# Optimization experiments

Hardware: AMD Instinct MI355X
Metric: run time of the kernel (lower is better)

## Reference

```python
import jax, jax.numpy as jnp
import numpy as np

SP_NEAR = 2
BN_EPS = 1e-5


def setup_inputs() -> dict:
    key = jax.random.key(0)
    ks = jax.random.split(key, 8)
    bs, n_stk, n_stk_pnt, coord = 32, 32, 64, 32
    sp_in, sp_out, dn_in, dn_out = 1024, 512, 256, 128
    return {
        "sparse_fea": jax.random.normal(ks[0], (bs, sp_in, n_stk), jnp.float32),
        "dense_fea": jax.random.normal(ks[1], (bs, dn_in, n_stk, n_stk_pnt), jnp.float32),
        "stk_coor": jax.random.normal(ks[2], (bs, n_stk, coord), jnp.float32),
        "stk_coor_bef": jax.random.normal(ks[3], (bs, 2 * n_stk, coord), jnp.float32),
        "sp_w": jax.random.normal(ks[4], (sp_out, sp_in), jnp.float32) * 0.02,
        "sp_b": jnp.zeros((sp_out,), jnp.float32),
        "sp_gamma": jnp.ones((sp_out,), jnp.float32),
        "sp_beta": jnp.zeros((sp_out,), jnp.float32),
        "ct_w": jax.random.normal(ks[5], (dn_in, dn_out, 1, 4), jnp.float32) * 0.02,  # torch ConvTranspose2d layout [in,out,kh,kw]
        "ct_b": jnp.zeros((dn_out,), jnp.float32),
        "bn_gamma": jnp.ones((dn_out,), jnp.float32),
        "bn_beta": jnp.zeros((dn_out,), jnp.float32),
    }


def reference(sparse_fea, dense_fea, stk_coor, stk_coor_bef,
              sp_w, sp_b, sp_gamma, sp_beta, ct_w, ct_b, bn_gamma, bn_beta):
    bs, dn_in, n_stk, n_stk_pnt = dense_fea.shape
    n_bef = stk_coor_bef.shape[1]  # n_stk * 2

    # ---- squared pairwise distances [bs, n_bef, n_stk] (eu.square_distance) ----
    d = (jnp.sum(stk_coor_bef ** 2, -1)[:, :, None]
         + jnp.sum(stk_coor ** 2, -1)[:, None, :]
         - 2.0 * jnp.einsum('bnc,bmc->bnm', stk_coor_bef, stk_coor))

    # ---- k smallest distances (sort + slice == top_k of -d) ----
    neg_d, idx = jax.lax.top_k(-d, SP_NEAR)  # idx: [bs, n_bef, 2]
    dists = -neg_d

    # ---- inverse-distance interpolation weights ----
    dist_recip = 1.0 / (dists + 1e-8)
    weight = dist_recip / jnp.sum(dist_recip, axis=2, keepdims=True)  # [bs, n_bef, 2]

    # ---- sparse branch: gather [bs, c, n_bef, 2] then weighted sum over neighbors ----
    sp_g = jax.vmap(lambda f, i: f[:, i])(sparse_fea, idx)  # [bs, sp_in, n_bef, 2]
    sp_interp = jnp.einsum('bcnk,bnk->bcn', sp_g, weight)   # [bs, sp_in, n_bef]

    # eu.MLP(dim=1): Conv1d(k=1) + BatchNorm1d (batch stats) + ReLU (dropout = identity)
    h = jnp.einsum('oc,bcn->bon', sp_w, sp_interp) + sp_b[None, :, None]
    mu = h.mean(axis=(0, 2), keepdims=True)
    var = h.var(axis=(0, 2), keepdims=True)
    sparse_out = jax.nn.relu(sp_gamma[None, :, None] * (h - mu) * jax.lax.rsqrt(var + BN_EPS)
                             + sp_beta[None, :, None])

    # ---- dense branch: rearrange 'b c s sp -> b s (sp c)', gather, weighted sum ----
    dflat = jnp.transpose(dense_fea, (0, 2, 3, 1)).reshape(bs, n_stk, n_stk_pnt * dn_in)
    dg = jax.vmap(lambda f, i: f[i])(dflat, idx)            # [bs, n_bef, 2, sp*c]
    dsum = jnp.einsum('bnkd,bnk->bnd', dg, weight)          # [bs, n_bef, sp*c]
    dense = jnp.transpose(dsum.reshape(bs, n_bef, n_stk_pnt, dn_in), (0, 3, 1, 2))  # [bs,c,n_bef,sp]

    # ---- ConvTranspose2d k=(1,4), s=(1,2), p=(0,1) as lhs-dilated conv with flipped kernel ----
    w_conv = jnp.flip(jnp.transpose(ct_w, (1, 0, 2, 3)), axis=(2, 3))  # [out,in,1,4]
    y = jax.lax.conv_general_dilated(
        dense, w_conv, window_strides=(1, 1),
        padding=((0, 0), (2, 2)),  # kh-1-0=0, kw-1-1=2
        lhs_dilation=(1, 2),
        dimension_numbers=('NCHW', 'OIHW', 'NCHW')) + ct_b[None, :, None, None]

    # BatchNorm2d (batch stats) + ReLU (Dropout2d = identity)
    mu2 = y.mean(axis=(0, 2, 3), keepdims=True)
    var2 = y.var(axis=(0, 2, 3), keepdims=True)
    dense_out = jax.nn.relu(bn_gamma[None, :, None, None] * (y - mu2) * jax.lax.rsqrt(var2 + BN_EPS)
                            + bn_beta[None, :, None, None])

    return sparse_out, dense_out
```

## Files before the change

### kernel.cpp

```cpp
#include <hip/hip_runtime.h>
#include <hip/hip_bf16.h>

typedef __attribute__((ext_vector_type(8))) short short8;
typedef __attribute__((ext_vector_type(4))) float f32x4;
typedef __attribute__((ext_vector_type(16))) float f32x16;

#define MFMA16(a,b,c) __builtin_amdgcn_mfma_f32_16x16x32_bf16((a),(b),(c),0,0,0)
#define MFMA32(a,b,c) __builtin_amdgcn_mfma_f32_32x32x16_bf16((a),(b),(c),0,0,0)

static __device__ __forceinline__ float b2f(ushort u){
  union { unsigned u32; float f; } x; x.u32 = ((unsigned)u) << 16; return x.f;
}
static __device__ __forceinline__ unsigned cvt2(float lo, float hi){
  unsigned r; asm("v_cvt_pk_bf16_f32 %0, %1, %2" : "=v"(r) : "v"(lo), "v"(hi)); return r;
}
static __device__ __forceinline__ ushort f2b1(float f){
  unsigned r; asm("v_cvt_pk_bf16_f32 %0, %1, %2" : "=v"(r) : "v"(f), "v"(f));
  return (ushort)r;
}
static __device__ __forceinline__ float relu(float v){ return (v <= 0.f) ? 0.f : v; }

__global__ __launch_bounds__(256) void k_knn(const float* __restrict__ bef,
    const float* __restrict__ coor, int* __restrict__ idx, float* __restrict__ wgt,
    float* __restrict__ stats){
  int blk = blockIdx.x, tid = threadIdx.x;
  if(blk == 0){
    for(int j = tid; j < 1280; j += 256) stats[j] = 0.f;
  }
  int t = blk*256 + tid;
  int b = t >> 6;
  float v[32]; float sb = 0.f;
  const float* br = bef + (size_t)t * 32;
  #pragma unroll
  for(int c=0;c<32;c++){ float x = br[c]; v[c] = x; sb += x*x; }
  float d0 = 1e30f, d1 = 1e30f; int i0 = 0, i1 = 0;
  const float* cr = coor + (size_t)b * 1024;
  for(int m=0;m<32;m++){
    float dot = 0.f, sc = 0.f;
    #pragma unroll
    for(int c=0;c<32;c++){ float x = cr[m*32+c]; dot += v[c]*x; sc += x*x; }
    float d = sb + sc - 2.f*dot;
    if(d < d0){ d1 = d0; i1 = i0; d0 = d; i0 = m; }
    else if(d < d1){ d1 = d; i1 = m; }
  }
  float r0 = 1.f/(d0 + 1e-8f), r1 = 1.f/(d1 + 1e-8f);
  float sum = r0 + r1;
  idx[t*2] = i0; idx[t*2+1] = i1;
  wgt[t*2] = r0/sum; wgt[t*2+1] = r1/sum;
}

__global__ __launch_bounds__(256) void k_prep(
    const float* __restrict__ spw, ushort* __restrict__ spwb,
    const float* __restrict__ ctw, ushort* __restrict__ Aev, ushort* __restrict__ Aod,
    const float* __restrict__ sf, const int* __restrict__ idx,
    const float* __restrict__ wgt, ushort* __restrict__ spiT){
  __shared__ float Ls[128*33];
  int blk = blockIdx.x, tid = threadIdx.x;
  if(blk < 512){
    int i = blk*256 + tid;
    int o = i >> 8;
    int k = (i & 255) * 4;
    float4 v = ((const float4*)spw)[i];
    uint2 ov; ov.x = cvt2(v.x, v.y); ov.y = cvt2(v.z, v.w);
    *(uint2*)(spwb + (size_t)(k>>3)*4096 + o*8 + (k&7)) = ov;
  } else if(blk < 768){
    int i = (blk-512)*256 + tid;
    int o = i >> 9, kc = i & 511;
    int c = kc & 255, hi = kc >> 8;
    const float* w = ctw + ((size_t)c*128 + o)*4;
    int j = ((kc>>3)<<10) + (o<<3) + (kc&7);
    Aev[j] = f2b1(w[hi ? 3 : 1]);
    Aod[j] = f2b1(w[hi ? 2 : 0]);
  } else {
    int blk2 = blk - 768;
    int b = blk2 >> 3, c0 = (blk2 & 7) * 128;
    const float* src = sf + (size_t)b*32768 + (size_t)c0*32;
    #pragma unroll
    for(int it=0; it<4; ++it){
      int q = it*256 + tid;
      int c = q >> 3, m = (q & 7)*4;
      float4 v = *(const float4*)(src + c*32 + m);
      Ls[c*33+m] = v.x; Ls[c*33+m+1] = v.y; Ls[c*33+m+2] = v.z; Ls[c*33+m+3] = v.w;
    }
    __syncthreads();
    int n = tid & 63, ob = tid >> 6;
    int bn = b*64 + n;
    int i0 = idx[bn*2], i1 = idx[bn*2+1];
    float w0 = wgt[bn*2], w1 = wgt[bn*2+1];
    ushort* dst = spiT + (size_t)b*65536 + n*8;
    #pragma unroll
    for(int it=0; it<4; ++it){
      int oct = ob + it*4;
      float f[8];
      #pragma unroll
      for(int j=0;j<8;j++){
        int c = oct*8 + j;
        f[j] = w0*Ls[c*33+i0] + w1*Ls[c*33+i1];
      }
      uint4 uv; uv.x = cvt2(f[0],f[1]); uv.y = cvt2(f[2],f[3]);
      uv.z = cvt2(f[4],f[5]); uv.w = cvt2(f[6],f[7]);
      *(uint4*)(dst + (size_t)((c0>>3) + oct)*512) = uv;
    }
  }
}

__global__ __launch_bounds__(256) void k_main(
    const ushort* __restrict__ spw, const ushort* __restrict__ spiT,
    const float* __restrict__ spb, float* __restrict__ h, float* __restrict__ sstats,
    const float* __restrict__ df, const ushort* __restrict__ Aev,
    const ushort* __restrict__ Aod, const float* __restrict__ ctb,
    ushort* __restrict__ z){
  __shared__ ushort L[66*256];
  int tid = threadIdx.x;
  int wave = tid >> 6, lane = tid & 63;

  if(blockIdx.x < 512){
    int blk = blockIdx.x;
    int b = blk >> 4, og = (blk >> 1) & 7, nh = blk & 1;
    int lo = lane & 15, hi = lane >> 4;
    int o0 = og*64 + wave*16;
    const short* A = (const short*)spw  + (size_t)hi*4096 + (o0 + lo)*8;
    const short* B = (const short*)spiT + (size_t)b*65536 + (size_t)hi*512 + (nh*32 + lo)*8;
    f32x4 acc[2] = {};
    for(int kb = 0; kb < 128; kb += 4){
      short8 a = *(const short8*)(A + (size_t)kb*4096);
      acc[0] = MFMA16(a, *(const short8*)(B + (size_t)kb*512),       acc[0]);
      acc[1] = MFMA16(a, *(const short8*)(B + (size_t)kb*512 + 128), acc[1]);
    }
    float sv[4], sv2[4], bias[4];
    #pragma unroll
    for(int r=0;r<4;r++){ sv[r]=0.f; sv2[r]=0.f; bias[r] = spb[o0 + hi*4 + r]; }
    #pragma unroll
    for(int q=0;q<2;q++){
      int n = nh*32 + q*16 + lo;
      #pragma unroll
      for(int r=0;r<4;r++){
        int o = o0 + hi*4 + r;
        float val = acc[q][r] + bias[r];
        h[(size_t)o*2048 + b*64 + n] = val;
        sv[r] += val; sv2[r] += val*val;
      }
    }
    #pragma unroll
    for(int r=0;r<4;r++){
      #pragma unroll
      for(int off=1; off<16; off<<=1){
        sv[r]  += __shfl_xor(sv[r],  off);
        sv2[r] += __shfl_xor(sv2[r], off);
      }
    }
    if(lo == 0){
      #pragma unroll
      for(int r=0;r<4;r++){
        int o = o0 + hi*4 + r;
        atomicAdd(&sstats[o*2],   sv[r]);
        atomicAdd(&sstats[o*2+1], sv2[r]);
      }
    }
    return;
  }

  int bs_ = blockIdx.x - 512; int b = bs_ >> 5, s = bs_ & 31;
  {
    unsigned* Lw = (unsigned*)L;
    int i = (tid < 128) ? tid : (65*128 + (tid - 128));
    Lw[i] = 0u;
  }
  {
    int p = tid & 63;
    const float* src = df + ((size_t)(b*256)*32 + s)*64 + p;
    int row = p + 1;
    char* Lrow = (char*)L + row*512;
    int rsw = row & 31;
    #pragma unroll
    for(int it=0; it<8; ++it){
      int oct = (tid >> 6) + it*4;
      const float* sc = src + (size_t)oct*8*2048;
      float f[8];
      #pragma unroll
      for(int j=0;j<8;j++) f[j] = sc[(size_t)j*2048];
      uint4 uv; uv.x = cvt2(f[0],f[1]); uv.y = cvt2(f[2],f[3]);
      uv.z = cvt2(f[4],f[5]); uv.w = cvt2(f[6],f[7]);
      *(uint4*)(Lrow + ((oct ^ rsw) << 4)) = uv;
    }
  }
  __syncthreads();

  int pe = wave >> 1, tt = wave & 1;
  int tcol = lane & 31;
  int t = tt*32 + tcol;
  int kl = (lane >> 5) * 8;
  const short* A = (const short*)(pe ? Aod : Aev) + (size_t)(lane>>5)*1024 + tcol*8;
  f32x16 acc[4] = {};
  #pragma unroll
  for(int hf=0; hf<2; ++hf){
    int rowr = t + (hf==0 ? 1 : 0) + pe;
    const char* Lr = (const char*)L + rowr*512;
    int rsw = rowr & 31;
    for(int k0=0; k0<256; k0+=16){
      int sidx = (k0 + kl) >> 3;
      short8 bfrag = *(const short8*)(Lr + ((sidx ^ rsw) << 4));
      const short* Ab = A + (size_t)((hf*256 + k0) >> 3)*1024;
      #pragma unroll
      for(int ot=0; ot<4; ++ot){
        short8 afrag = *(const short8*)(Ab + ot*256);
        acc[ot] = MFMA32(afrag, bfrag, acc[ot]);
      }
    }
  }
  __syncthreads();

  #pragma unroll
  for(int ot=0; ot<4; ++ot){
    #pragma unroll
    for(int r=0;r<16;r++){
      int o = ot*32 + (r&3) + 8*(r>>2) + 4*(lane>>5);
      L[o*128 + 2*t + pe] = f2b1(acc[ot][r] + ctb[o]);
    }
  }
  __syncthreads();
  ushort* zb = z + ((size_t)(b*128)*32 + s)*128;
  #pragma unroll
  for(int it=0; it<8; ++it){
    int q = it*256 + tid;
    int o = q >> 4, w0 = (q & 15)*8;
    *(short8*)(zb + (size_t)o*4096 + w0) = *(const short8*)(L + o*128 + w0);
  }
}

__global__ __launch_bounds__(256) void k_mid(const float* __restrict__ h,
    const float* __restrict__ sstats, const float* __restrict__ gam,
    const float* __restrict__ bet, float* __restrict__ out,
    const ushort* __restrict__ z, const int* __restrict__ idx,
    const float* __restrict__ wgt, float* __restrict__ dstats){
  __shared__ float ps[4], ps2[4];
  int blk = blockIdx.x, tid = threadIdx.x;
  if(blk < 512){
    int o = blk;
    float mu = sstats[o*2] / 2048.f;
    float var = fmaxf(sstats[o*2+1] / 2048.f - mu*mu, 0.f);
    float a = gam[o] * rsqrtf(var + 1e-5f);
    float be = bet[o];
    const float* row = h + (size_t)o * 2048;
    #pragma unroll
    for(int it=0; it<2; ++it){
      int j = it*1024 + tid*4;
      float4 v = *(const float4*)(row + j);
      float4 r;
      r.x = relu(a*(v.x-mu)+be); r.y = relu(a*(v.y-mu)+be);
      r.z = relu(a*(v.z-mu)+be); r.w = relu(a*(v.w-mu)+be);
      int b = j >> 6, n = j & 63;
      *(float4*)(out + ((size_t)b*512 + o)*64 + n) = r;
    }
  } else {
    int t = blk - 512; int b = t >> 7, o = t & 127;
    const uint2* zq = (const uint2*)(z + (size_t)(b*128 + o) * 4096);
    int wq = tid & 31, ng = tid >> 5;
    float s = 0.f, s2 = 0.f;
    for(int n = ng; n < 64; n += 8){
      int bn = b*64 + n;
      float w0 = wgt[bn*2], w1 = wgt[bn*2+1];
      int i0 = idx[bn*2], i1 = idx[bn*2+1];
      uint2 a0 = zq[i0*32 + wq], a1 = zq[i1*32 + wq];
      float y0 = w0*b2f((ushort)a0.x)       + w1*b2f((ushort)a1.x);
      float y1 = w0*b2f((ushort)(a0.x>>16)) + w1*b2f((ushort)(a1.x>>16));
      float y2 = w0*b2f((ushort)a0.y)       + w1*b2f((ushort)a1.y);
      float y3 = w0*b2f((ushort)(a0.y>>16)) + w1*b2f((ushort)(a1.y>>16));
      s  += y0+y1+y2+y3;
      s2 += y0*y0+y1*y1+y2*y2+y3*y3;
    }
    #pragma unroll
    for(int off=32; off; off>>=1){ s += __shfl_down(s, off); s2 += __shfl_down(s2, off); }
    int wave = tid >> 6, lane = tid & 63;
    if(lane == 0){ ps[wave] = s; ps2[wave] = s2; }
    __syncthreads();
    if(tid == 0){
      atomicAdd(&dstats[o*2],   ps[0]+ps[1]+ps[2]+ps[3]);
      atomicAdd(&dstats[o*2+1], ps2[0]+ps2[1]+ps2[2]+ps2[3]);
    }
  }
}

__global__ __launch_bounds__(256) void k_dout(const ushort* __restrict__ z,
    const int* __restrict__ idx, const float* __restrict__ wgt,
    const float* __restrict__ stats, const float* __restrict__ gam,
    const float* __restrict__ bet, float* __restrict__ out){
  int blk = blockIdx.x; int b = blk >> 7, o = blk & 127;
  const float N = 262144.f;
  float mu = stats[o*2] / N;
  float var = fmaxf(stats[o*2+1] / N - mu*mu, 0.f);
  float a = gam[o] * rsqrtf(var + 1e-5f);
  float be = bet[o];
  const uint2* zq = (const uint2*)(z + (size_t)(b*128 + o) * 4096);
  float* ob = out + 1048576 + (size_t)(b*128 + o) * 8192;
  int tid = threadIdx.x, wq = tid & 31, ng = tid >> 5;
  for(int n = ng; n < 64; n += 8){
    int bn = b*64 + n;
    float w0 = wgt[bn*2], w1 = wgt[bn*2+1];
    int i0 = idx[bn*2], i1 = idx[bn*2+1];
    uint2 a0 = zq[i0*32 + wq], a1 = zq[i1*32 + wq];
    float y0 = w0*b2f((ushort)a0.x)       + w1*b2f((ushort)a1.x);
    float y1 = w0*b2f((ushort)(a0.x>>16)) + w1*b2f((ushort)(a1.x>>16));
    float y2 = w0*b2f((ushort)a0.y)       + w1*b2f((ushort)a1.y);
    float y3 = w0*b2f((ushort)(a0.y>>16)) + w1*b2f((ushort)(a1.y>>16));
    float4 r;
    r.x = relu(a*(y0-mu)+be); r.y = relu(a*(y1-mu)+be);
    r.z = relu(a*(y2-mu)+be); r.w = relu(a*(y3-mu)+be);
    *(float4*)(ob + n*128 + wq*4) = r;
  }
}

extern "C" void kernel_launch(void* const* d_in, const int* in_sizes, int n_in,
                              void* d_out, int out_size, void* d_ws, size_t ws_size,
                              hipStream_t stream) {
  (void)in_sizes; (void)n_in; (void)out_size; (void)ws_size;
  const float* sparse_fea = (const float*)d_in[0];
  const float* dense_fea  = (const float*)d_in[1];
  const float* stk_coor   = (const float*)d_in[2];
  const float* stk_bef    = (const float*)d_in[3];
  const float* sp_w   = (const float*)d_in[4];
  const float* sp_b   = (const float*)d_in[5];
  const float* sp_g   = (const float*)d_in[6];
  const float* sp_be  = (const float*)d_in[7];
  const float* ct_w   = (const float*)d_in[8];
  const float* ct_b   = (const float*)d_in[9];
  const float* bn_g   = (const float*)d_in[10];
  const float* bn_be  = (const float*)d_in[11];
  float* out = (float*)d_out;

  char* ws = (char*)d_ws;
  int*    idx    = (int*)   (ws + 0);
  float*  wgt    = (float*) (ws + 16384);
  float*  sstats = (float*) (ws + 32768);
  float*  dstats = (float*) (ws + 36864);
  ushort* Aev    = (ushort*)(ws + 40960);
  ushort* Aod    = (ushort*)(ws + 172032);
  ushort* spwb   = (ushort*)(ws + 303104);
  ushort* spiT   = (ushort*)(ws + 1351680);
  float*  h      = (float*) (ws + 5545984);
  ushort* z      = (ushort*)(ws + 9740288);

  hipLaunchKernelGGL(k_knn,  dim3(8),    dim3(256), 0, stream,
                     stk_bef, stk_coor, idx, wgt, sstats);
  hipLaunchKernelGGL(k_prep, dim3(1024), dim3(256), 0, stream,
                     sp_w, spwb, ct_w, Aev, Aod, sparse_fea, idx, wgt, spiT);
  hipLaunchKernelGGL(k_main, dim3(1536), dim3(256), 0, stream,
                     spwb, spiT, sp_b, h, sstats, dense_fea, Aev, Aod, ct_b, z);
  hipLaunchKernelGGL(k_mid,  dim3(4608), dim3(256), 0, stream,
                     h, sstats, sp_g, sp_be, out, z, idx, wgt, dstats);
  hipLaunchKernelGGL(k_dout, dim3(4096), dim3(256), 0, stream,
                     z, idx, wgt, dstats, bn_g, bn_be, out);
}
```

Measured before the change: 160.3 us.

## Fuse kNN into prep kernel and widen z gather loads to 128-bit

Removes the separate kNN launch. Each sparse-gather block of the prep kernel now recomputes the kNN for its batch redundantly (all 256 threads compute it, and 64 store it to shared memory), and the block with c0==0 also writes idx and wgt to global for later kernels. Stats zeroing moves into block 512. The dense stats and output kernels now load uint4 (8 bf16) per thread instead of uint2, halving the load instruction count. The trade is redundant kNN compute (8x per batch, 4x per block) against one fewer launch and serial dependency.

Result: faster. 137.9 us (-14.0%).

```diff
diff --git a/kernel.cpp b/kernel.cpp
--- a/kernel.cpp
+++ b/kernel.cpp
@@ -20,41 +20,15 @@
 }
 static __device__ __forceinline__ float relu(float v){ return (v <= 0.f) ? 0.f : v; }
 
-__global__ __launch_bounds__(256) void k_knn(const float* __restrict__ bef,
-    const float* __restrict__ coor, int* __restrict__ idx, float* __restrict__ wgt,
-    float* __restrict__ stats){
-  int blk = blockIdx.x, tid = threadIdx.x;
-  if(blk == 0){
-    for(int j = tid; j < 1280; j += 256) stats[j] = 0.f;
-  }
-  int t = blk*256 + tid;
-  int b = t >> 6;
-  float v[32]; float sb = 0.f;
-  const float* br = bef + (size_t)t * 32;
-  #pragma unroll
-  for(int c=0;c<32;c++){ float x = br[c]; v[c] = x; sb += x*x; }
-  float d0 = 1e30f, d1 = 1e30f; int i0 = 0, i1 = 0;
-  const float* cr = coor + (size_t)b * 1024;
-  for(int m=0;m<32;m++){
-    float dot = 0.f, sc = 0.f;
-    #pragma unroll
-    for(int c=0;c<32;c++){ float x = cr[m*32+c]; dot += v[c]*x; sc += x*x; }
-    float d = sb + sc - 2.f*dot;
-    if(d < d0){ d1 = d0; i1 = i0; d0 = d; i0 = m; }
-    else if(d < d1){ d1 = d; i1 = m; }
-  }
-  float r0 = 1.f/(d0 + 1e-8f), r1 = 1.f/(d1 + 1e-8f);
-  float sum = r0 + r1;
-  idx[t*2] = i0; idx[t*2+1] = i1;
-  wgt[t*2] = r0/sum; wgt[t*2+1] = r1/sum;
-}
-
 __global__ __launch_bounds__(256) void k_prep(
     const float* __restrict__ spw, ushort* __restrict__ spwb,
     const float* __restrict__ ctw, ushort* __restrict__ Aev, ushort* __restrict__ Aod,
-    const float* __restrict__ sf, const int* __restrict__ idx,
-    const float* __restrict__ wgt, ushort* __restrict__ spiT){
+    const float* __restrict__ sf, const float* __restrict__ bef,
+    const float* __restrict__ coor, int* __restrict__ idx, float* __restrict__ wgt,
+    ushort* __restrict__ spiT, float* __restrict__ stats){
   __shared__ float Ls[128*33];
+  __shared__ float kw0[64], kw1[64];
+  __shared__ int   ki0[64], ki1[64];
   int blk = blockIdx.x, tid = threadIdx.x;
   if(blk < 512){
     int i = blk*256 + tid;
@@ -64,6 +38,9 @@
     uint2 ov; ov.x = cvt2(v.x, v.y); ov.y = cvt2(v.z, v.w);
     *(uint2*)(spwb + (size_t)(k>>3)*4096 + o*8 + (k&7)) = ov;
   } else if(blk < 768){
+    if(blk == 512){
+      for(int j = tid; j < 1280; j += 256) stats[j] = 0.f;
+    }
     int i = (blk-512)*256 + tid;
     int o = i >> 9, kc = i & 511;
     int c = kc & 255, hi = kc >> 8;
@@ -82,11 +59,38 @@
       float4 v = *(const float4*)(src + c*32 + m);
       Ls[c*33+m] = v.x; Ls[c*33+m+1] = v.y; Ls[c*33+m+2] = v.z; Ls[c*33+m+3] = v.w;
     }
+    {
+      int n = tid & 63;
+      int t = b*64 + n;
+      float v[32]; float sb = 0.f;
+      const float* br = bef + (size_t)t * 32;
+      #pragma unroll
+      for(int c=0;c<32;c++){ float x = br[c]; v[c] = x; sb += x*x; }
+      float d0 = 1e30f, d1 = 1e30f; int i0 = 0, i1 = 0;
+      const float* cr = coor + (size_t)b * 1024;
+      for(int m=0;m<32;m++){
+        float dot = 0.f, sc = 0.f;
+        #pragma unroll
+        for(int c=0;c<32;c++){ float x = cr[m*32+c]; dot += v[c]*x; sc += x*x; }
+        float d = sb + sc - 2.f*dot;
+        if(d < d0){ d1 = d0; i1 = i0; d0 = d; i0 = m; }
+        else if(d < d1){ d1 = d; i1 = m; }
+      }
+      float r0 = 1.f/(d0 + 1e-8f), r1 = 1.f/(d1 + 1e-8f);
+      float sum = r0 + r1;
+      if(tid < 64){
+        ki0[n] = i0; ki1[n] = i1;
+        kw0[n] = r0/sum; kw1[n] = r1/sum;
+        if(c0 == 0){
+          idx[t*2] = i0; idx[t*2+1] = i1;
+          wgt[t*2] = r0/sum; wgt[t*2+1] = r1/sum;
+        }
+      }
+    }
     __syncthreads();
     int n = tid & 63, ob = tid >> 6;
-    int bn = b*64 + n;
-    int i0 = idx[bn*2], i1 = idx[bn*2+1];
-    float w0 = wgt[bn*2], w1 = wgt[bn*2+1];
+    int i0 = ki0[n], i1 = ki1[n];
+    float w0 = kw0[n], w1 = kw1[n];
     ushort* dst = spiT + (size_t)b*65536 + n*8;
     #pragma unroll
     for(int it=0; it<4; ++it){
@@ -254,20 +258,21 @@
     }
   } else {
     int t = blk - 512; int b = t >> 7, o = t & 127;
-    const uint2* zq = (const uint2*)(z + (size_t)(b*128 + o) * 4096);
-    int wq = tid & 31, ng = tid >> 5;
+    const uint4* zq = (const uint4*)(z + (size_t)(b*128 + o) * 4096);
+    int wq = tid & 15, ng = tid >> 4;
     float s = 0.f, s2 = 0.f;
-    for(int n = ng; n < 64; n += 8){
+    for(int n = ng; n < 64; n += 16){
       int bn = b*64 + n;
       float w0 = wgt[bn*2], w1 = wgt[bn*2+1];
       int i0 = idx[bn*2], i1 = idx[bn*2+1];
-      uint2 a0 = zq[i0*32 + wq], a1 = zq[i1*32 + wq];
-      float y0 = w0*b2f((ushort)a0.x)       + w1*b2f((ushort)a1.x);
-      float y1 = w0*b2f((ushort)(a0.x>>16)) + w1*b2f((ushort)(a1.x>>16));
-      float y2 = w0*b2f((ushort)a0.y)       + w1*b2f((ushort)a1.y);
-      float y3 = w0*b2f((ushort)(a0.y>>16)) + w1*b2f((ushort)(a1.y>>16));
-      s  += y0+y1+y2+y3;
-      s2 += y0*y0+y1*y1+y2*y2+y3*y3;
+      uint4 a0 = zq[i0*16 + wq], a1 = zq[i1*16 + wq];
+      #pragma unroll
+      for(int j=0;j<4;j++){
+        unsigned u0 = (&a0.x)[j], u1 = (&a1.x)[j];
+        float y0 = w0*b2f((ushort)u0)       + w1*b2f((ushort)u1);
+        float y1 = w0*b2f((ushort)(u0>>16)) + w1*b2f((ushort)(u1>>16));
+        s += y0 + y1; s2 += y0*y0 + y1*y1;
+      }
     }
     #pragma unroll
     for(int off=32; off; off>>=1){ s += __shfl_down(s, off); s2 += __shfl_down(s2, off); }
@@ -291,22 +296,28 @@
   float var = fmaxf(stats[o*2+1] / N - mu*mu, 0.f);
   float a = gam[o] * rsqrtf(var + 1e-5f);
   float be = bet[o];
-  const uint2* zq = (const uint2*)(z + (size_t)(b*128 + o) * 4096);
+  const uint4* zq = (const uint4*)(z + (size_t)(b*128 + o) * 4096);
   float* ob = out + 1048576 + (size_t)(b*128 + o) * 8192;
-  int tid = threadIdx.x, wq = tid & 31, ng = tid >> 5;
-  for(int n = ng; n < 64; n += 8){
+  int tid = threadIdx.x, wq = tid & 15, ng = tid >> 4;
+  for(int n = ng; n < 64; n += 16){
     int bn = b*64 + n;
     float w0 = wgt[bn*2], w1 = wgt[bn*2+1];
     int i0 = idx[bn*2], i1 = idx[bn*2+1];
-    uint2 a0 = zq[i0*32 + wq], a1 = zq[i1*32 + wq];
-    float y0 = w0*b2f((ushort)a0.x)       + w1*b2f((ushort)a1.x);
-    float y1 = w0*b2f((ushort)(a0.x>>16)) + w1*b2f((ushort)(a1.x>>16));
-    float y2 = w0*b2f((ushort)a0.y)       + w1*b2f((ushort)a1.y);
-    float y3 = w0*b2f((ushort)(a0.y>>16)) + w1*b2f((ushort)(a1.y>>16));
-    float4 r;
-    r.x = relu(a*(y0-mu)+be); r.y = relu(a*(y1-mu)+be);
-    r.z = relu(a*(y2-mu)+be); r.w = relu(a*(y3-mu)+be);
-    *(float4*)(ob + n*128 + wq*4) = r;
+    uint4 a0 = zq[i0*16 + wq], a1 = zq[i1*16 + wq];
+    float y[8];
+    #pragma unroll
+    for(int j=0;j<4;j++){
+      unsigned u0 = (&a0.x)[j], u1 = (&a1.x)[j];
+      y[2*j]   = w0*b2f((ushort)u0)       + w1*b2f((ushort)u1);
+      y[2*j+1] = w0*b2f((ushort)(u0>>16)) + w1*b2f((ushort)(u1>>16));
+    }
+    float4 r0, r1;
+    r0.x = relu(a*(y[0]-mu)+be); r0.y = relu(a*(y[1]-mu)+be);
+    r0.z = relu(a*(y[2]-mu)+be); r0.w = relu(a*(y[3]-mu)+be);
+    r1.x = relu(a*(y[4]-mu)+be); r1.y = relu(a*(y[5]-mu)+be);
+    r1.z = relu(a*(y[6]-mu)+be); r1.w = relu(a*(y[7]-mu)+be);
+    *(float4*)(ob + n*128 + wq*8)     = r0;
+    *(float4*)(ob + n*128 + wq*8 + 4) = r1;
   }
 }
 
@@ -340,10 +351,9 @@
   float*  h      = (float*) (ws + 5545984);
   ushort* z      = (ushort*)(ws + 9740288);
 
-  hipLaunchKernelGGL(k_knn,  dim3(8),    dim3(256), 0, stream,
-                     stk_bef, stk_coor, idx, wgt, sstats);
   hipLaunchKernelGGL(k_prep, dim3(1024), dim3(256), 0, stream,
-                     sp_w, spwb, ct_w, Aev, Aod, sparse_fea, idx, wgt, spiT);
+                     sp_w, spwb, ct_w, Aev, Aod, sparse_fea, stk_bef, stk_coor,
+                     idx, wgt, spiT, sstats);
   hipLaunchKernelGGL(k_main, dim3(1536), dim3(256), 0, stream,
                      spwb, spiT, sp_b, h, sstats, dense_fea, Aev, Aod, ct_b, z);
   hipLaunchKernelGGL(k_mid,  dim3(4608), dim3(256), 0, stream,
```
